# Kernel tuning notes

Hardware: AMD Instinct MI355X
Metric: run time of the kernel (lower is better)

The kernel has to match this reference:

```python
import jax, jax.numpy as jnp
import numpy as np

N_NODES = 50000
N_EDGES = 400000
D_PROT = 512
D_TEXT = 2048
GN_EPS = 1e-5


def setup_inputs() -> dict:
    key = jax.random.key(0)
    ks = jax.random.split(key, 8)
    s = 0.02
    return {
        "x": jax.random.normal(ks[0], (N_NODES, D_PROT), jnp.float32),
        "edge_index": jax.random.randint(ks[1], (2, N_EDGES), 0, N_NODES, dtype=jnp.int32),
        "gn_weight": jnp.ones((D_PROT,), jnp.float32),
        "gn_bias": jnp.zeros((D_PROT,), jnp.float32),
        "gn_mean_scale": jnp.ones((D_PROT,), jnp.float32),
        "conv1_w": jax.random.normal(ks[2], (D_PROT, D_PROT), jnp.float32) * s,
        "conv1_b": jnp.zeros((D_PROT,), jnp.float32),
        "conv2_w": jax.random.normal(ks[3], (D_PROT, D_PROT), jnp.float32) * s,
        "conv2_b": jnp.zeros((D_PROT,), jnp.float32),
        "proj1_w": jax.random.normal(ks[4], (D_TEXT, D_PROT), jnp.float32) * s,
        "proj1_b": jnp.zeros((D_TEXT,), jnp.float32),
        "proj2_w": jax.random.normal(ks[5], (D_TEXT, D_TEXT), jnp.float32) * s,
        "proj2_b": jnp.zeros((D_TEXT,), jnp.float32),
    }


def _graph_norm(x, weight, bias, mean_scale):
    # PyG GraphNorm over a single graph: shift by mean_scale*mean, scale by rstd
    mean = jnp.mean(x, axis=0, keepdims=True)            # [1, D]
    out = x - mean * mean_scale
    var = jnp.mean(out * out, axis=0, keepdims=True)     # [1, D]
    out = out * jax.lax.rsqrt(var + GN_EPS)
    return out * weight + bias


def _sgconv(x, src, dst, w, b):
    # SGConv K=1 with GCN normalization and added self-loops:
    n = x.shape[0]
    deg = jax.ops.segment_sum(jnp.ones_like(src, dtype=x.dtype), dst, num_segments=n) + 1.0
    dinv = jax.lax.rsqrt(deg)                            # [N]
    norm = dinv[src] * dinv[dst]                         # [E]
    agg = jax.ops.segment_sum(x[src] * norm[:, None], dst, num_segments=n)
    agg = agg + x * (dinv * dinv)[:, None]               # self-loop contribution
    return agg @ w.T + b


def reference(x, edge_index, gn_weight, gn_bias, gn_mean_scale,
              conv1_w, conv1_b, conv2_w, conv2_b,
              proj1_w, proj1_b, proj2_w, proj2_b):
    src, dst = edge_index[0], edge_index[1]
    h = _graph_norm(x, gn_weight, gn_bias, gn_mean_scale)
    h = jax.nn.relu(_sgconv(h, src, dst, conv1_w, conv1_b))  # dropout = identity (eval)
    h = jax.nn.relu(_sgconv(h, src, dst, conv2_w, conv2_b))
    h = h @ proj1_w.T + proj1_b
    h = jax.nn.gelu(h, approximate=False)
    h = h @ proj2_w.T + proj2_b
    return h
```

## Files before the change

### kernel.cpp

```cpp
#include <hip/hip_runtime.h>
#include <math.h>

typedef _Float16 half_t;
typedef _Float16 f16x2 __attribute__((ext_vector_type(2)));
typedef _Float16 f16x4 __attribute__((ext_vector_type(4)));
typedef _Float16 f16x8 __attribute__((ext_vector_type(8)));
typedef float f32x4 __attribute__((ext_vector_type(4)));

#define D_PROT 512
#define D_TEXT 2048

__global__ void k_cvt4(const float* __restrict__ s, half_t* __restrict__ d, int n4) {
    int i = blockIdx.x * 256 + threadIdx.x;
    if (i < n4) {
        float4 v = ((const float4*)s)[i];
        f16x4 o;
        o.x = (_Float16)v.x; o.y = (_Float16)v.y;
        o.z = (_Float16)v.z; o.w = (_Float16)v.w;
        ((f16x4*)d)[i] = o;
    }
}

__global__ void k_deg(const int* __restrict__ dst, int E, int* __restrict__ deg) {
    int i = blockIdx.x * 256 + threadIdx.x;
    if (i < E) atomicAdd(&deg[dst[i]], 1);
}

__global__ void k_dinv(const int* __restrict__ deg, float* __restrict__ dinv, int n) {
    int i = blockIdx.x * 256 + threadIdx.x;
    if (i < n) dinv[i] = rsqrtf((float)deg[i] + 1.0f);
}

__global__ void k_blocksum(const int* __restrict__ deg, int* __restrict__ bsum, int n) {
    __shared__ int sd[256];
    int i = blockIdx.x * 256 + threadIdx.x;
    sd[threadIdx.x] = (i < n) ? deg[i] : 0;
    __syncthreads();
    for (int s = 128; s > 0; s >>= 1) {
        if (threadIdx.x < s) sd[threadIdx.x] += sd[threadIdx.x + s];
        __syncthreads();
    }
    if (threadIdx.x == 0) bsum[blockIdx.x] = sd[0];
}

__global__ void k_scan_bsum(const int* __restrict__ bsum, int* __restrict__ boff, int nb) {
    __shared__ int sd[1024];
    int t = threadIdx.x;
    for (int i = t; i < 1024; i += 256) sd[i] = (i < nb) ? bsum[i] : 0;
    __syncthreads();
    for (int s = 1; s < 1024; s <<= 1) {
        int vals[4];
#pragma unroll
        for (int k = 0; k < 4; k++) {
            int i = t + k * 256;
            vals[k] = (i >= s) ? sd[i - s] : 0;
        }
        __syncthreads();
#pragma unroll
        for (int k = 0; k < 4; k++) sd[t + k * 256] += vals[k];
        __syncthreads();
    }
    for (int i = t; i < nb; i += 256) boff[i] = (i > 0) ? sd[i - 1] : 0;
}

__global__ void k_scan_final(const int* __restrict__ deg, const int* __restrict__ boff,
                             int* __restrict__ rowptr, int n) {
    __shared__ int sd[256];
    int i = blockIdx.x * 256 + threadIdx.x;
    int v = (i < n) ? deg[i] : 0;
    sd[threadIdx.x] = v;
    __syncthreads();
    for (int s = 1; s < 256; s <<= 1) {
        int t2 = (threadIdx.x >= s) ? sd[threadIdx.x - s] : 0;
        __syncthreads();
        sd[threadIdx.x] += t2;
        __syncthreads();
    }
    if (i < n) rowptr[i + 1] = boff[blockIdx.x] + sd[threadIdx.x];
}

__global__ void k_fill(const int* __restrict__ src, const int* __restrict__ dst, int E,
                       const int* __restrict__ rowptr, int* __restrict__ fill,
                       int* __restrict__ colidx) {
    int i = blockIdx.x * 256 + threadIdx.x;
    if (i < E) {
        int d = dst[i];
        int pos = atomicAdd(&fill[d], 1);
        colidx[rowptr[d] + pos] = src[i];
    }
}

__global__ void k_gnreduce(const float* __restrict__ x, float* __restrict__ sums,
                           float* __restrict__ sumsq, int Nn) {
    int t = threadIdx.x;
    int c = t * 2;
    float s0 = 0, s1 = 0, q0 = 0, q1 = 0;
    for (int r = blockIdx.x; r < Nn; r += gridDim.x) {
        float2 v = *(const float2*)(x + (size_t)r * D_PROT + c);
        s0 += v.x; s1 += v.y; q0 += v.x * v.x; q1 += v.y * v.y;
    }
    atomicAdd(&sums[c], s0);  atomicAdd(&sums[c + 1], s1);
    atomicAdd(&sumsq[c], q0); atomicAdd(&sumsq[c + 1], q1);
}

__global__ void k_gnfinal(const float* __restrict__ sums, const float* __restrict__ sumsq,
                          const float* __restrict__ w, const float* __restrict__ b,
                          const float* __restrict__ ms, float* __restrict__ ab, float invN) {
    int d = blockIdx.x * 256 + threadIdx.x;
    if (d < D_PROT) {
        float mean = sums[d] * invN;
        float m2 = sumsq[d] * invN;
        float mm = mean * ms[d];
        float var = m2 - 2.f * mm * mean + mm * mm;
        float rstd = rsqrtf(var + 1e-5f);
        float a = rstd * w[d];
        ab[d] = a;
        ab[D_PROT + d] = b[d] - mm * a;
    }
}

__global__ void k_gnnorm(const float* __restrict__ x, const float* __restrict__ ab,
                         half_t* __restrict__ h, int n4) {
    int i = blockIdx.x * 256 + threadIdx.x;
    if (i < n4) {
        size_t idx = (size_t)i * 4;
        float4 v = *(const float4*)(x + idx);
        int d = (int)(idx & (D_PROT - 1));
        const float* a = ab;
        const float* bb = ab + D_PROT;
        f16x4 o;
        o.x = (_Float16)(v.x * a[d]     + bb[d]);
        o.y = (_Float16)(v.y * a[d + 1] + bb[d + 1]);
        o.z = (_Float16)(v.z * a[d + 2] + bb[d + 2]);
        o.w = (_Float16)(v.w * a[d + 3] + bb[d + 3]);
        *(f16x4*)(h + idx) = o;
    }
}

__global__ void k_agg(const half_t* __restrict__ h, half_t* __restrict__ out,
                      const int* __restrict__ rowptr, const int* __restrict__ colidx,
                      const float* __restrict__ dinv, int Nn) {
    int wid = (blockIdx.x << 2) + (threadIdx.x >> 6);
    if (wid >= Nn) return;
    int lane = threadIdx.x & 63;
    int node = wid;
    float di = dinv[node];
    int beg = rowptr[node], end = rowptr[node + 1];
    const f16x8* hp = (const f16x8*)h;
    f16x8 sv = hp[(size_t)node * 64 + lane];
    float dii = di * di;
    float a[8];
#pragma unroll
    for (int j = 0; j < 8; j++) a[j] = (float)sv[j] * dii;
    int e = beg;
    for (; e + 4 <= end; e += 4) {
        int s0 = colidx[e],     s1 = colidx[e + 1];
        int s2 = colidx[e + 2], s3 = colidx[e + 3];
        float w0 = dinv[s0] * di, w1 = dinv[s1] * di;
        float w2 = dinv[s2] * di, w3 = dinv[s3] * di;
        f16x8 v0 = hp[(size_t)s0 * 64 + lane];
        f16x8 v1 = hp[(size_t)s1 * 64 + lane];
        f16x8 v2 = hp[(size_t)s2 * 64 + lane];
        f16x8 v3 = hp[(size_t)s3 * 64 + lane];
#pragma unroll
        for (int j = 0; j < 8; j++)
            a[j] += w0 * (float)v0[j] + w1 * (float)v1[j]
                  + w2 * (float)v2[j] + w3 * (float)v3[j];
    }
    for (; e < end; ++e) {
        int s = colidx[e];
        float wg = dinv[s] * di;
        f16x8 v = hp[(size_t)s * 64 + lane];
#pragma unroll
        for (int j = 0; j < 8; j++) a[j] += wg * (float)v[j];
    }
    f16x8 o;
#pragma unroll
    for (int j = 0; j < 8; j++) o[j] = (_Float16)a[j];
    ((f16x8*)out)[(size_t)node * 64 + lane] = o;
}

#define FENCE() asm volatile("" ::: "memory")
#define BAR()   do { FENCE(); __builtin_amdgcn_s_barrier(); FENCE(); } while (0)
#define WAITV4() asm volatile("s_waitcnt vmcnt(4)" ::: "memory")
#define WAITV0() asm volatile("s_waitcnt vmcnt(0)" ::: "memory")
#define GLD(src, dst) __builtin_amdgcn_global_load_lds( \
    (const __attribute__((address_space(1))) void*)(src), \
    (__attribute__((address_space(3))) void*)(dst), 16, 0, 0)
#define LDF(base, row, kk) \
    (*(const f16x8*)((base) + ((((row) * 128 + (kk) * 64 + fqo)) ^ (((row) & 7) << 4))))
#define MM(mi, nj, A_, B_) \
    acc[mi][nj] = __builtin_amdgcn_mfma_f32_16x16x32_f16(A_, B_, acc[mi][nj], 0, 0, 0)

template <int ACT, typename OUT_T>
__global__ __launch_bounds__(512, 2) void k_gemm8(const half_t* __restrict__ A,
                                                  const half_t* __restrict__ W,
                                                  const float* __restrict__ bias,
                                                  OUT_T* __restrict__ C,
                                                  int M, int N, int K) {
    __shared__ half_t sm[2][32768];
    const int gx = gridDim.x;
    const int nwg = gx * gridDim.y;
    int b = blockIdx.y * gx + blockIdx.x;
    int w8 = ((nwg & 7) == 0) ? (b & 7) * (nwg >> 3) + (b >> 3) : b;
    const int bn = (w8 % gx) * 256;
    const int bm = (w8 / gx) * 256;

    const int t = threadIdx.x;
    const int w = t >> 6, lane = t & 63;
    const int fr = lane & 15, fq = lane >> 4;
    const int fqo = fq * 16;
    const int wm = (w >> 2) * 128, wn = (w & 3) * 64;
    const int NT = K >> 6;

    int q0 = w * 512 + lane * 8;
    int q1 = 4096 + q0;
    int s0 = q0 ^ (((q0 >> 6) & 7) << 3);
    int s1 = q1 ^ (((q1 >> 6) & 7) << 3);
    int r0 = s0 >> 6, c0 = s0 & 63;
    int r1 = s1 >> 6, c1 = s1 & 63;
    const half_t* gAlo0 = A + (size_t)min(bm + r0, M - 1) * K + c0;
    const half_t* gAlo1 = A + (size_t)min(bm + r1, M - 1) * K + c1;
    const half_t* gAhi0 = A + (size_t)min(bm + 128 + r0, M - 1) * K + c0;
    const half_t* gAhi1 = A + (size_t)min(bm + 128 + r1, M - 1) * K + c1;
    const half_t* gBlo0 = W + (size_t)(bn + r0) * K + c0;
    const half_t* gBlo1 = W + (size_t)(bn + r1) * K + c1;
    const half_t* gBhi0 = W + (size_t)(bn + 128 + r0) * K + c0;
    const half_t* gBhi1 = W + (size_t)(bn + 128 + r1) * K + c1;
    const int dst0 = w * 512;

    f32x4 acc[8][4] = {};

    GLD(gAlo0, &sm[0][dst0]);          GLD(gAlo1, &sm[0][4096 + dst0]);
    GLD(gAhi0, &sm[0][8192 + dst0]);   GLD(gAhi1, &sm[0][12288 + dst0]);
    GLD(gBlo0, &sm[0][16384 + dst0]);  GLD(gBlo1, &sm[0][20480 + dst0]);
    GLD(gBhi0, &sm[0][24576 + dst0]);  GLD(gBhi1, &sm[0][28672 + dst0]);
    GLD(gBlo0 + 64, &sm[1][16384 + dst0]);  GLD(gBlo1 + 64, &sm[1][20480 + dst0]);
    GLD(gBhi0 + 64, &sm[1][24576 + dst0]);  GLD(gBhi1 + 64, &sm[1][28672 + dst0]);
    WAITV4();
    BAR();

#define TILE(cur, nxt, ktA, ktB) do {                                          \
    const char* smA = (const char*)&sm[cur][0];                                 \
    const char* smB = (const char*)&sm[cur][16384];                             \
                  \
    f16x8 b00 = LDF(smB, wn + fr, 0),      b01 = LDF(smB, wn + fr, 1);          \
    f16x8 b10 = LDF(smB, wn + 16 + fr, 0), b11 = LDF(smB, wn + 16 + fr, 1);     \
    f16x8 b20 = LDF(smB, wn + 32 + fr, 0), b21 = LDF(smB, wn + 32 + fr, 1);     \
    f16x8 b30 = LDF(smB, wn + 48 + fr, 0), b31 = LDF(smB, wn + 48 + fr, 1);     \
    f16x8 a00 = LDF(smA, wm + fr, 0),      a01 = LDF(smA, wm + fr, 1);          \
    f16x8 a10 = LDF(smA, wm + 16 + fr, 0), a11 = LDF(smA, wm + 16 + fr, 1);     \
    GLD(gAlo0 + (size_t)(ktA) * 64, &sm[nxt][dst0]);                            \
    GLD(gAlo1 + (size_t)(ktA) * 64, &sm[nxt][4096 + dst0]);                     \
    GLD(gAhi0 + (size_t)(ktA) * 64, &sm[nxt][8192 + dst0]);                     \
    GLD(gAhi1 + (size_t)(ktA) * 64, &sm[nxt][12288 + dst0]);                    \
    BAR();                                                                      \
    __builtin_amdgcn_s_setprio(1);                                              \
    MM(0, 0, a00, b00); MM(0, 1, a00, b10); MM(0, 2, a00, b20); MM(0, 3, a00, b30); \
    MM(0, 0, a01, b01); MM(0, 1, a01, b11); MM(0, 2, a01, b21); MM(0, 3, a01, b31); \
    MM(1, 0, a10, b00); MM(1, 1, a10, b10); MM(1, 2, a10, b20); MM(1, 3, a10, b30); \
    MM(1, 0, a11, b01); MM(1, 1, a11, b11); MM(1, 2, a11, b21); MM(1, 3, a11, b31); \
    __builtin_amdgcn_s_setprio(0);                                              \
    BAR();                                                                      \
                              \
    f16x8 a20 = LDF(smA, wm + 32 + fr, 0), a21 = LDF(smA, wm + 32 + fr, 1);     \
    f16x8 a30 = LDF(smA, wm + 48 + fr, 0), a31 = LDF(smA, wm + 48 + fr, 1);     \
    GLD(gBlo0 + (size_t)(ktB) * 64, &sm[cur][16384 + dst0]);                    \
    GLD(gBlo1 + (size_t)(ktB) * 64, &sm[cur][20480 + dst0]);                    \
    BAR();                                                                      \
    __builtin_amdgcn_s_setprio(1);                                              \
    MM(2, 0, a20, b00); MM(2, 1, a20, b10); MM(2, 2, a20, b20); MM(2, 3, a20, b30); \
    MM(2, 0, a21, b01); MM(2, 1, a21, b11); MM(2, 2, a21, b21); MM(2, 3, a21, b31); \
    MM(3, 0, a30, b00); MM(3, 1, a30, b10); MM(3, 2, a30, b20); MM(3, 3, a30, b30); \
    MM(3, 0, a31, b01); MM(3, 1, a31, b11); MM(3, 2, a31, b21); MM(3, 3, a31, b31); \
    __builtin_amdgcn_s_setprio(0);                                              \
    BAR();                                                                      \
                              \
    f16x8 a40 = LDF(smA, wm + 64 + fr, 0), a41 = LDF(smA, wm + 64 + fr, 1);     \
    f16x8 a50 = LDF(smA, wm + 80 + fr, 0), a51 = LDF(smA, wm + 80 + fr, 1);     \
    GLD(gBhi0 + (size_t)(ktB) * 64, &sm[cur][24576 + dst0]);                    \
    GLD(gBhi1 + (size_t)(ktB) * 64, &sm[cur][28672 + dst0]);                    \
    BAR();                                                                      \
    __builtin_amdgcn_s_setprio(1);                                              \
    MM(4, 0, a40, b00); MM(4, 1, a40, b10); MM(4, 2, a40, b20); MM(4, 3, a40, b30); \
    MM(4, 0, a41, b01); MM(4, 1, a41, b11); MM(4, 2, a41, b21); MM(4, 3, a41, b31); \
    MM(5, 0, a50, b00); MM(5, 1, a50, b10); MM(5, 2, a50, b20); MM(5, 3, a50, b30); \
    MM(5, 0, a51, b01); MM(5, 1, a51, b11); MM(5, 2, a51, b21); MM(5, 3, a51, b31); \
    __builtin_amdgcn_s_setprio(0);                                              \
    BAR();                                                                      \
                                       \
    f16x8 a60 = LDF(smA, wm + 96 + fr, 0),  a61 = LDF(smA, wm + 96 + fr, 1);    \
    f16x8 a70 = LDF(smA, wm + 112 + fr, 0), a71 = LDF(smA, wm + 112 + fr, 1);   \
    BAR();                                                                      \
    __builtin_amdgcn_s_setprio(1);                                              \
    MM(6, 0, a60, b00); MM(6, 1, a60, b10); MM(6, 2, a60, b20); MM(6, 3, a60, b30); \
    MM(6, 0, a61, b01); MM(6, 1, a61, b11); MM(6, 2, a61, b21); MM(6, 3, a61, b31); \
    MM(7, 0, a70, b00); MM(7, 1, a70, b10); MM(7, 2, a70, b20); MM(7, 3, a70, b30); \
    MM(7, 0, a71, b01); MM(7, 1, a71, b11); MM(7, 2, a71, b21); MM(7, 3, a71, b31); \
    __builtin_amdgcn_s_setprio(0);                                              \
    WAITV4();                                                                   \
    BAR();                                                                      \
} while (0)

    for (int tt = 0; tt < NT; tt += 2) {
        int kb1 = (tt + 2 < NT) ? tt + 2 : NT - 1;
        TILE(0, 1, tt + 1, kb1);
        int ka2 = (tt + 2 < NT) ? tt + 2 : NT - 1;
        int kb2 = (tt + 3 < NT) ? tt + 3 : NT - 1;
        TILE(1, 0, ka2, kb2);
    }
    WAITV0();
#undef TILE

    const int col0 = bn + wn + fr;
#pragma unroll
    for (int mi = 0; mi < 8; mi++) {
        int rb = bm + wm + mi * 16 + fq * 4;
#pragma unroll
        for (int nj = 0; nj < 4; nj++) {
            int col = col0 + nj * 16;
            float bv = bias[col];
#pragma unroll
            for (int r = 0; r < 4; r++) {
                int row = rb + r;
                if (row < M) {
                    float v = acc[mi][nj][r] + bv;
                    if (ACT == 1) v = fmaxf(v, 0.f);
                    if (ACT == 2) v = 0.5f * v * (1.f + erff(v * 0.70710678118f));
                    C[(size_t)row * N + col] = (OUT_T)v;
                }
            }
        }
    }
}

extern "C" void kernel_launch(void* const* d_in, const int* in_sizes, int n_in,
                              void* d_out, int out_size, void* d_ws, size_t ws_size,
                              hipStream_t stream) {
    const float* x     = (const float*)d_in[0];
    const int*   eidx  = (const int*)d_in[1];
    const float* gn_w  = (const float*)d_in[2];
    const float* gn_b  = (const float*)d_in[3];
    const float* gn_ms = (const float*)d_in[4];
    const float* w1    = (const float*)d_in[5];
    const float* b1    = (const float*)d_in[6];
    const float* w2    = (const float*)d_in[7];
    const float* b2    = (const float*)d_in[8];
    const float* p1    = (const float*)d_in[9];
    const float* pb1   = (const float*)d_in[10];
    const float* p2    = (const float*)d_in[11];
    const float* pb2   = (const float*)d_in[12];

    const int Nn = in_sizes[0] / D_PROT;
    const int E  = in_sizes[1] / 2;
    const int M  = Nn;

    char* ws = (char*)d_ws;
    size_t off = 0;
    auto alloc = [&](size_t bytes) {
        void* p = ws + off;
        off += (bytes + 255) & ~(size_t)255;
        return p;
    };
    half_t* w1h    = (half_t*)alloc((size_t)D_PROT * D_PROT * 2);
    half_t* w2h    = (half_t*)alloc((size_t)D_PROT * D_PROT * 2);
    half_t* p1h    = (half_t*)alloc((size_t)D_TEXT * D_PROT * 2);
    half_t* p2h    = (half_t*)alloc((size_t)D_TEXT * D_TEXT * 2);
    int*    deg    = (int*)alloc((size_t)Nn * 4);
    float*  dinv   = (float*)alloc((size_t)Nn * 4);
    int*    rowptr = (int*)alloc((size_t)(Nn + 1) * 4);
    int*    fillc  = (int*)alloc((size_t)Nn * 4);
    int*    bsum   = (int*)alloc(4096);
    int*    boff   = (int*)alloc(4096);
    int*    colidx = (int*)alloc((size_t)E * 4);
    float*  sums   = (float*)alloc(D_PROT * 4);
    float*  sumsq  = (float*)alloc(D_PROT * 4);
    float*  gnab   = (float*)alloc(2 * D_PROT * 4);
    half_t* buf1   = (half_t*)alloc((size_t)Nn * D_PROT * 2);
    half_t* buf2   = (half_t*)alloc((size_t)Nn * D_PROT * 2);
    half_t* big    = (half_t*)alloc((size_t)Nn * D_TEXT * 2);

    const int* esrc = eidx;
    const int* edst = eidx + E;

    hipMemsetAsync(deg, 0, (size_t)Nn * 4, stream);
    hipMemsetAsync(fillc, 0, (size_t)Nn * 4, stream);
    hipMemsetAsync(rowptr, 0, (size_t)(Nn + 1) * 4, stream);
    hipMemsetAsync(sums, 0, D_PROT * 4, stream);
    hipMemsetAsync(sumsq, 0, D_PROT * 4, stream);

    k_cvt4<<<(D_PROT * D_PROT / 4 + 255) / 256, 256, 0, stream>>>(w1, w1h, D_PROT * D_PROT / 4);
    k_cvt4<<<(D_PROT * D_PROT / 4 + 255) / 256, 256, 0, stream>>>(w2, w2h, D_PROT * D_PROT / 4);
    k_cvt4<<<(D_TEXT * D_PROT / 4 + 255) / 256, 256, 0, stream>>>(p1, p1h, D_TEXT * D_PROT / 4);
    k_cvt4<<<(D_TEXT * D_TEXT / 4 + 255) / 256, 256, 0, stream>>>(p2, p2h, D_TEXT * D_TEXT / 4);

    int eb = (E + 255) / 256;
    int nb = (Nn + 255) / 256;
    k_deg<<<eb, 256, 0, stream>>>(edst, E, deg);
    k_dinv<<<nb, 256, 0, stream>>>(deg, dinv, Nn);
    k_blocksum<<<nb, 256, 0, stream>>>(deg, bsum, Nn);
    k_scan_bsum<<<1, 256, 0, stream>>>(bsum, boff, nb);
    k_scan_final<<<nb, 256, 0, stream>>>(deg, boff, rowptr, Nn);
    k_fill<<<eb, 256, 0, stream>>>(esrc, edst, E, rowptr, fillc, colidx);

    k_gnreduce<<<256, 256, 0, stream>>>(x, sums, sumsq, Nn);
    k_gnfinal<<<2, 256, 0, stream>>>(sums, sumsq, gn_w, gn_b, gn_ms, gnab, 1.0f / (float)Nn);
    int n4 = Nn * D_PROT / 4;
    k_gnnorm<<<(n4 + 255) / 256, 256, 0, stream>>>(x, gnab, buf1, n4);

    const int mt256 = (M + 255) / 256;
    const int aggb = (Nn + 3) / 4;

    k_agg<<<aggb, 256, 0, stream>>>(buf1, buf2, rowptr, colidx, dinv, Nn);
    {
        dim3 g(D_PROT / 256, mt256);
        k_gemm8<1, half_t><<<g, 512, 0, stream>>>(buf2, w1h, b1, buf1, M, D_PROT, D_PROT);
    }
    k_agg<<<aggb, 256, 0, stream>>>(buf1, buf2, rowptr, colidx, dinv, Nn);
    {
        dim3 g(D_PROT / 256, mt256);
        k_gemm8<1, half_t><<<g, 512, 0, stream>>>(buf2, w2h, b2, buf1, M, D_PROT, D_PROT);
    }
    {
        dim3 g(D_TEXT / 256, mt256);
        k_gemm8<2, half_t><<<g, 512, 0, stream>>>(buf1, p1h, pb1, big, M, D_TEXT, D_PROT);
    }
    {
        dim3 g(D_TEXT / 256, mt256);
        k_gemm8<0, float><<<g, 512, 0, stream>>>(big, p2h, pb2, (float*)d_out, M, D_TEXT, D_TEXT);
    }
}
```

Baseline: 1.249 ms.

## Restructure GEMM to 256x128 tiles with K=32 triple-buffered LDS pipeline

Rewrites the fp16 MFMA GEMM from 256x256 tiles with K=64 double buffering to 256x128 tiles with K=32 steps and a three-stage LDS ring. It uses a new swizzle, a simpler per-iteration loop with one barrier, and a column-major workgroup order that walks M inside each N strip. Less LDS per block and launch_bounds raised to 4 are meant to give higher occupancy and a deeper prefetch. In exchange, each block reuses less data per MFMA and B tiles are reloaded more often, so global and LDS traffic per FLOP rises.

```diff
diff --git a/kernel.cpp b/kernel.cpp
--- a/kernel.cpp
+++ b/kernel.cpp
@@ -2,7 +2,6 @@
 #include <math.h>
 
 typedef _Float16 half_t;
-typedef _Float16 f16x2 __attribute__((ext_vector_type(2)));
 typedef _Float16 f16x4 __attribute__((ext_vector_type(4)));
 typedef _Float16 f16x8 __attribute__((ext_vector_type(8)));
 typedef float f32x4 __attribute__((ext_vector_type(4)));
@@ -182,149 +181,97 @@
 
 #define FENCE() asm volatile("" ::: "memory")
 #define BAR()   do { FENCE(); __builtin_amdgcn_s_barrier(); FENCE(); } while (0)
-#define WAITV4() asm volatile("s_waitcnt vmcnt(4)" ::: "memory")
+#define WAITV3() asm volatile("s_waitcnt vmcnt(3)" ::: "memory")
 #define WAITV0() asm volatile("s_waitcnt vmcnt(0)" ::: "memory")
 #define GLD(src, dst) __builtin_amdgcn_global_load_lds( \
     (const __attribute__((address_space(1))) void*)(src), \
     (__attribute__((address_space(3))) void*)(dst), 16, 0, 0)
-#define LDF(base, row, kk) \
-    (*(const f16x8*)((base) + ((((row) * 128 + (kk) * 64 + fqo)) ^ (((row) & 7) << 4))))
+#define LDF(base, row) \
+    (*(const f16x8*)((base) + ((((row) * 64 + fqo)) ^ ((((row) >> 1) & 3) << 4))))
 #define MM(mi, nj, A_, B_) \
     acc[mi][nj] = __builtin_amdgcn_mfma_f32_16x16x32_f16(A_, B_, acc[mi][nj], 0, 0, 0)
 
 template <int ACT, typename OUT_T>
-__global__ __launch_bounds__(512, 2) void k_gemm8(const half_t* __restrict__ A,
+__global__ __launch_bounds__(512, 4) void k_gemm8(const half_t* __restrict__ A,
                                                   const half_t* __restrict__ W,
                                                   const float* __restrict__ bias,
                                                   OUT_T* __restrict__ C,
                                                   int M, int N, int K) {
-    __shared__ half_t sm[2][32768];
+    __shared__ half_t sm[36864];
     const int gx = gridDim.x;
-    const int nwg = gx * gridDim.y;
+    const int mt = gridDim.y;
+    const int nwg = gx * mt;
     int b = blockIdx.y * gx + blockIdx.x;
     int w8 = ((nwg & 7) == 0) ? (b & 7) * (nwg >> 3) + (b >> 3) : b;
-    const int bn = (w8 % gx) * 256;
-    const int bm = (w8 / gx) * 256;
+    const int bn = (w8 / mt) * 128;
+    const int bm = (w8 % mt) * 256;
 
     const int t = threadIdx.x;
     const int w = t >> 6, lane = t & 63;
     const int fr = lane & 15, fq = lane >> 4;
     const int fqo = fq * 16;
-    const int wm = (w >> 2) * 128, wn = (w & 3) * 64;
-    const int NT = K >> 6;
-
-    int q0 = w * 512 + lane * 8;
-    int q1 = 4096 + q0;
-    int s0 = q0 ^ (((q0 >> 6) & 7) << 3);
-    int s1 = q1 ^ (((q1 >> 6) & 7) << 3);
-    int r0 = s0 >> 6, c0 = s0 & 63;
-    int r1 = s1 >> 6, c1 = s1 & 63;
-    const half_t* gAlo0 = A + (size_t)min(bm + r0, M - 1) * K + c0;
-    const half_t* gAlo1 = A + (size_t)min(bm + r1, M - 1) * K + c1;
-    const half_t* gAhi0 = A + (size_t)min(bm + 128 + r0, M - 1) * K + c0;
-    const half_t* gAhi1 = A + (size_t)min(bm + 128 + r1, M - 1) * K + c1;
-    const half_t* gBlo0 = W + (size_t)(bn + r0) * K + c0;
-    const half_t* gBlo1 = W + (size_t)(bn + r1) * K + c1;
-    const half_t* gBhi0 = W + (size_t)(bn + 128 + r0) * K + c0;
-    const half_t* gBhi1 = W + (size_t)(bn + 128 + r1) * K + c1;
+    const int wm = (w >> 1) * 64, wn = (w & 1) * 64;
+    const int NT = K >> 5;
+
+    int q = w * 512 + lane * 8;
+    int s = q ^ (((q >> 6) & 3) << 3);
+    int r = s >> 5, c = s & 31;
+    const half_t* gAlo = A + (size_t)min(bm + r, M - 1) * K + c;
+    const half_t* gAhi = A + (size_t)min(bm + 128 + r, M - 1) * K + c;
+    const half_t* gB   = W + (size_t)(bn + r) * K + c;
     const int dst0 = w * 512;
 
-    f32x4 acc[8][4] = {};
-
-    GLD(gAlo0, &sm[0][dst0]);          GLD(gAlo1, &sm[0][4096 + dst0]);
-    GLD(gAhi0, &sm[0][8192 + dst0]);   GLD(gAhi1, &sm[0][12288 + dst0]);
-    GLD(gBlo0, &sm[0][16384 + dst0]);  GLD(gBlo1, &sm[0][20480 + dst0]);
-    GLD(gBhi0, &sm[0][24576 + dst0]);  GLD(gBhi1, &sm[0][28672 + dst0]);
-    GLD(gBlo0 + 64, &sm[1][16384 + dst0]);  GLD(gBlo1 + 64, &sm[1][20480 + dst0]);
-    GLD(gBhi0 + 64, &sm[1][24576 + dst0]);  GLD(gBhi1 + 64, &sm[1][28672 + dst0]);
-    WAITV4();
+#define STAGE(b3, kt) do {                                                     \
+    GLD(gB   + (size_t)(kt) * 32, &sm[(b3) * 12288 + 8192 + dst0]);            \
+    GLD(gAlo + (size_t)(kt) * 32, &sm[(b3) * 12288 + dst0]);                   \
+    GLD(gAhi + (size_t)(kt) * 32, &sm[(b3) * 12288 + 4096 + dst0]);            \
+} while (0)
+
+    f32x4 acc[4][4] = {};
+
+    STAGE(0, 0);
+    STAGE(1, (NT > 1) ? 1 : 0);
+    WAITV3();
     BAR();
 
-#define TILE(cur, nxt, ktA, ktB) do {                                          \
-    const char* smA = (const char*)&sm[cur][0];                                 \
-    const char* smB = (const char*)&sm[cur][16384];                             \
-                  \
-    f16x8 b00 = LDF(smB, wn + fr, 0),      b01 = LDF(smB, wn + fr, 1);          \
-    f16x8 b10 = LDF(smB, wn + 16 + fr, 0), b11 = LDF(smB, wn + 16 + fr, 1);     \
-    f16x8 b20 = LDF(smB, wn + 32 + fr, 0), b21 = LDF(smB, wn + 32 + fr, 1);     \
-    f16x8 b30 = LDF(smB, wn + 48 + fr, 0), b31 = LDF(smB, wn + 48 + fr, 1);     \
-    f16x8 a00 = LDF(smA, wm + fr, 0),      a01 = LDF(smA, wm + fr, 1);          \
-    f16x8 a10 = LDF(smA, wm + 16 + fr, 0), a11 = LDF(smA, wm + 16 + fr, 1);     \
-    GLD(gAlo0 + (size_t)(ktA) * 64, &sm[nxt][dst0]);                            \
-    GLD(gAlo1 + (size_t)(ktA) * 64, &sm[nxt][4096 + dst0]);                     \
-    GLD(gAhi0 + (size_t)(ktA) * 64, &sm[nxt][8192 + dst0]);                     \
-    GLD(gAhi1 + (size_t)(ktA) * 64, &sm[nxt][12288 + dst0]);                    \
-    BAR();                                                                      \
-    __builtin_amdgcn_s_setprio(1);                                              \
-    MM(0, 0, a00, b00); MM(0, 1, a00, b10); MM(0, 2, a00, b20); MM(0, 3, a00, b30); \
-    MM(0, 0, a01, b01); MM(0, 1, a01, b11); MM(0, 2, a01, b21); MM(0, 3, a01, b31); \
-    MM(1, 0, a10, b00); MM(1, 1, a10, b10); MM(1, 2, a10, b20); MM(1, 3, a10, b30); \
-    MM(1, 0, a11, b01); MM(1, 1, a11, b11); MM(1, 2, a11, b21); MM(1, 3, a11, b31); \
-    __builtin_amdgcn_s_setprio(0);                                              \
-    BAR();                                                                      \
-                              \
-    f16x8 a20 = LDF(smA, wm + 32 + fr, 0), a21 = LDF(smA, wm + 32 + fr, 1);     \
-    f16x8 a30 = LDF(smA, wm + 48 + fr, 0), a31 = LDF(smA, wm + 48 + fr, 1);     \
-    GLD(gBlo0 + (size_t)(ktB) * 64, &sm[cur][16384 + dst0]);                    \
-    GLD(gBlo1 + (size_t)(ktB) * 64, &sm[cur][20480 + dst0]);                    \
-    BAR();                                                                      \
-    __builtin_amdgcn_s_setprio(1);                                              \
-    MM(2, 0, a20, b00); MM(2, 1, a20, b10); MM(2, 2, a20, b20); MM(2, 3, a20, b30); \
-    MM(2, 0, a21, b01); MM(2, 1, a21, b11); MM(2, 2, a21, b21); MM(2, 3, a21, b31); \
-    MM(3, 0, a30, b00); MM(3, 1, a30, b10); MM(3, 2, a30, b20); MM(3, 3, a30, b30); \
-    MM(3, 0, a31, b01); MM(3, 1, a31, b11); MM(3, 2, a31, b21); MM(3, 3, a31, b31); \
-    __builtin_amdgcn_s_setprio(0);                                              \
-    BAR();                                                                      \
-                              \
-    f16x8 a40 = LDF(smA, wm + 64 + fr, 0), a41 = LDF(smA, wm + 64 + fr, 1);     \
-    f16x8 a50 = LDF(smA, wm + 80 + fr, 0), a51 = LDF(smA, wm + 80 + fr, 1);     \
-    GLD(gBhi0 + (size_t)(ktB) * 64, &sm[cur][24576 + dst0]);                    \
-    GLD(gBhi1 + (size_t)(ktB) * 64, &sm[cur][28672 + dst0]);                    \
-    BAR();                                                                      \
-    __builtin_amdgcn_s_setprio(1);                                              \
-    MM(4, 0, a40, b00); MM(4, 1, a40, b10); MM(4, 2, a40, b20); MM(4, 3, a40, b30); \
-    MM(4, 0, a41, b01); MM(4, 1, a41, b11); MM(4, 2, a41, b21); MM(4, 3, a41, b31); \
-    MM(5, 0, a50, b00); MM(5, 1, a50, b10); MM(5, 2, a50, b20); MM(5, 3, a50, b30); \
-    MM(5, 0, a51, b01); MM(5, 1, a51, b11); MM(5, 2, a51, b21); MM(5, 3, a51, b31); \
-    __builtin_amdgcn_s_setprio(0);                                              \
-    BAR();                                                                      \
-                                       \
-    f16x8 a60 = LDF(smA, wm + 96 + fr, 0),  a61 = LDF(smA, wm + 96 + fr, 1);    \
-    f16x8 a70 = LDF(smA, wm + 112 + fr, 0), a71 = LDF(smA, wm + 112 + fr, 1);   \
-    BAR();                                                                      \
-    __builtin_amdgcn_s_setprio(1);                                              \
-    MM(6, 0, a60, b00); MM(6, 1, a60, b10); MM(6, 2, a60, b20); MM(6, 3, a60, b30); \
-    MM(6, 0, a61, b01); MM(6, 1, a61, b11); MM(6, 2, a61, b21); MM(6, 3, a61, b31); \
-    MM(7, 0, a70, b00); MM(7, 1, a70, b10); MM(7, 2, a70, b20); MM(7, 3, a70, b30); \
-    MM(7, 0, a71, b01); MM(7, 1, a71, b11); MM(7, 2, a71, b21); MM(7, 3, a71, b31); \
-    __builtin_amdgcn_s_setprio(0);                                              \
-    WAITV4();                                                                   \
-    BAR();                                                                      \
-} while (0)
-
-    for (int tt = 0; tt < NT; tt += 2) {
-        int kb1 = (tt + 2 < NT) ? tt + 2 : NT - 1;
-        TILE(0, 1, tt + 1, kb1);
-        int ka2 = (tt + 2 < NT) ? tt + 2 : NT - 1;
-        int kb2 = (tt + 3 < NT) ? tt + 3 : NT - 1;
-        TILE(1, 0, ka2, kb2);
+    for (int tt = 0; tt < NT; ++tt) {
+        const int cur = tt % 3;
+        const int s2 = (tt + 2) % 3;
+        const int kt = (tt + 2 < NT) ? tt + 2 : NT - 1;
+        const char* smA = (const char*)&sm[cur * 12288];
+        const char* smB = smA + 16384;
+        STAGE(s2, kt);
+        f16x8 b0 = LDF(smB, wn + fr);
+        f16x8 b1 = LDF(smB, wn + 16 + fr);
+        f16x8 b2 = LDF(smB, wn + 32 + fr);
+        f16x8 b3 = LDF(smB, wn + 48 + fr);
+        __builtin_amdgcn_s_setprio(1);
+#pragma unroll
+        for (int mi = 0; mi < 4; mi++) {
+            f16x8 a = LDF(smA, wm + mi * 16 + fr);
+            MM(mi, 0, a, b0); MM(mi, 1, a, b1);
+            MM(mi, 2, a, b2); MM(mi, 3, a, b3);
+        }
+        __builtin_amdgcn_s_setprio(0);
+        WAITV3();
+        BAR();
     }
     WAITV0();
-#undef TILE
+#undef STAGE
 
     const int col0 = bn + wn + fr;
 #pragma unroll
-    for (int mi = 0; mi < 8; mi++) {
+    for (int mi = 0; mi < 4; mi++) {
         int rb = bm + wm + mi * 16 + fq * 4;
 #pragma unroll
         for (int nj = 0; nj < 4; nj++) {
             int col = col0 + nj * 16;
             float bv = bias[col];
 #pragma unroll
-            for (int r = 0; r < 4; r++) {
-                int row = rb + r;
+            for (int rr = 0; rr < 4; rr++) {
+                int row = rb + rr;
                 if (row < M) {
-                    float v = acc[mi][nj][r] + bv;
+                    float v = acc[mi][nj][rr] + bv;
                     if (ACT == 1) v = fmaxf(v, 0.f);
                     if (ACT == 2) v = 0.5f * v * (1.f + erff(v * 0.70710678118f));
                     C[(size_t)row * N + col] = (OUT_T)v;
@@ -413,20 +360,20 @@
 
     k_agg<<<aggb, 256, 0, stream>>>(buf1, buf2, rowptr, colidx, dinv, Nn);
     {
-        dim3 g(D_PROT / 256, mt256);
+        dim3 g(D_PROT / 128, mt256);
         k_gemm8<1, half_t><<<g, 512, 0, stream>>>(buf2, w1h, b1, buf1, M, D_PROT, D_PROT);
     }
     k_agg<<<aggb, 256, 0, stream>>>(buf1, buf2, rowptr, colidx, dinv, Nn);
     {
-        dim3 g(D_PROT / 256, mt256);
+        dim3 g(D_PROT / 128, mt256);
         k_gemm8<1, half_t><<<g, 512, 0, stream>>>(buf2, w2h, b2, buf1, M, D_PROT, D_PROT);
     }
     {
-        dim3 g(D_TEXT / 256, mt256);
+        dim3 g(D_TEXT / 128, mt256);
         k_gemm8<2, half_t><<<g, 512, 0, stream>>>(buf1, p1h, pb1, big, M, D_TEXT, D_PROT);
     }
     {
-        dim3 g(D_TEXT / 256, mt256);
+        dim3 g(D_TEXT / 128, mt256);
         k_gemm8<0, float><<<g, 512, 0, stream>>>(big, p2h, pb2, (float*)d_out, M, D_TEXT, D_TEXT);
     }
 }
```

After: 1.289 ms. 3.3% more time.

## Add 256x128 triple-buffered GEMM kernel for small-K layers

Applied to the files above, without the earlier changes.

Adds a new GEMM kernel with a 256x128 output tile, K-step of 32, a three-stage LDS ring buffer and launch bounds allowing four blocks per CU. It is used for the two 512x512 conv GEMMs and the 512->2048 projection, while the large 2048x2048 projection keeps the existing 256x256 kernel (renamed). The aim is more workgroups and better latency hiding when K is small, at the cost of lower per-tile data reuse and more barriers per unit of work.

```diff
diff --git a/kernel.cpp b/kernel.cpp
--- a/kernel.cpp
+++ b/kernel.cpp
@@ -2,7 +2,6 @@
 #include <math.h>
 
 typedef _Float16 half_t;
-typedef _Float16 f16x2 __attribute__((ext_vector_type(2)));
 typedef _Float16 f16x4 __attribute__((ext_vector_type(4)));
 typedef _Float16 f16x8 __attribute__((ext_vector_type(8)));
 typedef float f32x4 __attribute__((ext_vector_type(4)));
@@ -183,21 +182,23 @@
 #define FENCE() asm volatile("" ::: "memory")
 #define BAR()   do { FENCE(); __builtin_amdgcn_s_barrier(); FENCE(); } while (0)
 #define WAITV4() asm volatile("s_waitcnt vmcnt(4)" ::: "memory")
+#define WAITV3() asm volatile("s_waitcnt vmcnt(3)" ::: "memory")
 #define WAITV0() asm volatile("s_waitcnt vmcnt(0)" ::: "memory")
 #define GLD(src, dst) __builtin_amdgcn_global_load_lds( \
     (const __attribute__((address_space(1))) void*)(src), \
     (__attribute__((address_space(3))) void*)(dst), 16, 0, 0)
-#define LDF(base, row, kk) \
-    (*(const f16x8*)((base) + ((((row) * 128 + (kk) * 64 + fqo)) ^ (((row) & 7) << 4))))
 #define MM(mi, nj, A_, B_) \
     acc[mi][nj] = __builtin_amdgcn_mfma_f32_16x16x32_f16(A_, B_, acc[mi][nj], 0, 0, 0)
 
+#define LDF256(base, row, kk) \
+    (*(const f16x8*)((base) + ((((row) * 128 + (kk) * 64 + fqo)) ^ (((row) & 7) << 4))))
+
 template <int ACT, typename OUT_T>
-__global__ __launch_bounds__(512, 2) void k_gemm8(const half_t* __restrict__ A,
-                                                  const half_t* __restrict__ W,
-                                                  const float* __restrict__ bias,
-                                                  OUT_T* __restrict__ C,
-                                                  int M, int N, int K) {
+__global__ __launch_bounds__(512, 2) void k_gemm256(const half_t* __restrict__ A,
+                                                    const half_t* __restrict__ W,
+                                                    const float* __restrict__ bias,
+                                                    OUT_T* __restrict__ C,
+                                                    int M, int N, int K) {
     __shared__ half_t sm[2][32768];
     const int gx = gridDim.x;
     const int nwg = gx * gridDim.y;
@@ -243,13 +244,12 @@
 #define TILE(cur, nxt, ktA, ktB) do {                                          \
     const char* smA = (const char*)&sm[cur][0];                                 \
     const char* smB = (const char*)&sm[cur][16384];                             \
-                  \
-    f16x8 b00 = LDF(smB, wn + fr, 0),      b01 = LDF(smB, wn + fr, 1);          \
-    f16x8 b10 = LDF(smB, wn + 16 + fr, 0), b11 = LDF(smB, wn + 16 + fr, 1);     \
-    f16x8 b20 = LDF(smB, wn + 32 + fr, 0), b21 = LDF(smB, wn + 32 + fr, 1);     \
-    f16x8 b30 = LDF(smB, wn + 48 + fr, 0), b31 = LDF(smB, wn + 48 + fr, 1);     \
-    f16x8 a00 = LDF(smA, wm + fr, 0),      a01 = LDF(smA, wm + fr, 1);          \
-    f16x8 a10 = LDF(smA, wm + 16 + fr, 0), a11 = LDF(smA, wm + 16 + fr, 1);     \
+    f16x8 b00 = LDF256(smB, wn + fr, 0),      b01 = LDF256(smB, wn + fr, 1);    \
+    f16x8 b10 = LDF256(smB, wn + 16 + fr, 0), b11 = LDF256(smB, wn + 16 + fr, 1); \
+    f16x8 b20 = LDF256(smB, wn + 32 + fr, 0), b21 = LDF256(smB, wn + 32 + fr, 1); \
+    f16x8 b30 = LDF256(smB, wn + 48 + fr, 0), b31 = LDF256(smB, wn + 48 + fr, 1); \
+    f16x8 a00 = LDF256(smA, wm + fr, 0),      a01 = LDF256(smA, wm + fr, 1);    \
+    f16x8 a10 = LDF256(smA, wm + 16 + fr, 0), a11 = LDF256(smA, wm + 16 + fr, 1); \
     GLD(gAlo0 + (size_t)(ktA) * 64, &sm[nxt][dst0]);                            \
     GLD(gAlo1 + (size_t)(ktA) * 64, &sm[nxt][4096 + dst0]);                     \
     GLD(gAhi0 + (size_t)(ktA) * 64, &sm[nxt][8192 + dst0]);                     \
@@ -262,9 +262,8 @@
     MM(1, 0, a11, b01); MM(1, 1, a11, b11); MM(1, 2, a11, b21); MM(1, 3, a11, b31); \
     __builtin_amdgcn_s_setprio(0);                                              \
     BAR();                                                                      \
-                              \
-    f16x8 a20 = LDF(smA, wm + 32 + fr, 0), a21 = LDF(smA, wm + 32 + fr, 1);     \
-    f16x8 a30 = LDF(smA, wm + 48 + fr, 0), a31 = LDF(smA, wm + 48 + fr, 1);     \
+    f16x8 a20 = LDF256(smA, wm + 32 + fr, 0), a21 = LDF256(smA, wm + 32 + fr, 1); \
+    f16x8 a30 = LDF256(smA, wm + 48 + fr, 0), a31 = LDF256(smA, wm + 48 + fr, 1); \
     GLD(gBlo0 + (size_t)(ktB) * 64, &sm[cur][16384 + dst0]);                    \
     GLD(gBlo1 + (size_t)(ktB) * 64, &sm[cur][20480 + dst0]);                    \
     BAR();                                                                      \
@@ -275,9 +274,8 @@
     MM(3, 0, a31, b01); MM(3, 1, a31, b11); MM(3, 2, a31, b21); MM(3, 3, a31, b31); \
     __builtin_amdgcn_s_setprio(0);                                              \
     BAR();                                                                      \
-                              \
-    f16x8 a40 = LDF(smA, wm + 64 + fr, 0), a41 = LDF(smA, wm + 64 + fr, 1);     \
-    f16x8 a50 = LDF(smA, wm + 80 + fr, 0), a51 = LDF(smA, wm + 80 + fr, 1);     \
+    f16x8 a40 = LDF256(smA, wm + 64 + fr, 0), a41 = LDF256(smA, wm + 64 + fr, 1); \
+    f16x8 a50 = LDF256(smA, wm + 80 + fr, 0), a51 = LDF256(smA, wm + 80 + fr, 1); \
     GLD(gBhi0 + (size_t)(ktB) * 64, &sm[cur][24576 + dst0]);                    \
     GLD(gBhi1 + (size_t)(ktB) * 64, &sm[cur][28672 + dst0]);                    \
     BAR();                                                                      \
@@ -288,9 +286,8 @@
     MM(5, 0, a51, b01); MM(5, 1, a51, b11); MM(5, 2, a51, b21); MM(5, 3, a51, b31); \
     __builtin_amdgcn_s_setprio(0);                                              \
     BAR();                                                                      \
-                                       \
-    f16x8 a60 = LDF(smA, wm + 96 + fr, 0),  a61 = LDF(smA, wm + 96 + fr, 1);    \
-    f16x8 a70 = LDF(smA, wm + 112 + fr, 0), a71 = LDF(smA, wm + 112 + fr, 1);   \
+    f16x8 a60 = LDF256(smA, wm + 96 + fr, 0),  a61 = LDF256(smA, wm + 96 + fr, 1); \
+    f16x8 a70 = LDF256(smA, wm + 112 + fr, 0), a71 = LDF256(smA, wm + 112 + fr, 1); \
     BAR();                                                                      \
     __builtin_amdgcn_s_setprio(1);                                              \
     MM(6, 0, a60, b00); MM(6, 1, a60, b10); MM(6, 2, a60, b20); MM(6, 3, a60, b30); \
@@ -325,6 +322,98 @@
                 int row = rb + r;
                 if (row < M) {
                     float v = acc[mi][nj][r] + bv;
+                    if (ACT == 1) v = fmaxf(v, 0.f);
+                    if (ACT == 2) v = 0.5f * v * (1.f + erff(v * 0.70710678118f));
+                    C[(size_t)row * N + col] = (OUT_T)v;
+                }
+            }
+        }
+    }
+}
+
+#define LDF128(base, row) \
+    (*(const f16x8*)((base) + ((((row) * 64 + fqo)) ^ ((((row) >> 1) & 3) << 4))))
+
+template <int ACT, typename OUT_T>
+__global__ __launch_bounds__(512, 4) void k_gemm128(const half_t* __restrict__ A,
+                                                    const half_t* __restrict__ W,
+                                                    const float* __restrict__ bias,
+                                                    OUT_T* __restrict__ C,
+                                                    int M, int N, int K) {
+    __shared__ half_t sm[36864];
+    const int gx = gridDim.x;
+    const int nwg = gx * gridDim.y;
+    int b = blockIdx.y * gx + blockIdx.x;
+    int w8 = ((nwg & 7) == 0) ? (b & 7) * (nwg >> 3) + (b >> 3) : b;
+    const int bn = (w8 % gx) * 128;
+    const int bm = (w8 / gx) * 256;
+
+    const int t = threadIdx.x;
+    const int w = t >> 6, lane = t & 63;
+    const int fr = lane & 15, fq = lane >> 4;
+    const int fqo = fq * 16;
+    const int wm = (w >> 1) * 64, wn = (w & 1) * 64;
+    const int NT = K >> 5;
+
+    int q = w * 512 + lane * 8;
+    int s = q ^ (((q >> 6) & 3) << 3);
+    int r = s >> 5, c = s & 31;
+    const half_t* gAlo = A + (size_t)min(bm + r, M - 1) * K + c;
+    const half_t* gAhi = A + (size_t)min(bm + 128 + r, M - 1) * K + c;
+    const half_t* gB   = W + (size_t)(bn + r) * K + c;
+    const int dst0 = w * 512;
+
+#define STAGE(b3, kt) do {                                                     \
+    GLD(gB   + (size_t)(kt) * 32, &sm[(b3) * 12288 + 8192 + dst0]);            \
+    GLD(gAlo + (size_t)(kt) * 32, &sm[(b3) * 12288 + dst0]);                   \
+    GLD(gAhi + (size_t)(kt) * 32, &sm[(b3) * 12288 + 4096 + dst0]);            \
+} while (0)
+
+    f32x4 acc[4][4] = {};
+
+    STAGE(0, 0);
+    STAGE(1, (NT > 1) ? 1 : 0);
+    WAITV3();
+    BAR();
+
+    for (int tt = 0; tt < NT; ++tt) {
+        const int cur = tt % 3;
+        const int s2 = (tt + 2) % 3;
+        const int kt = (tt + 2 < NT) ? tt + 2 : NT - 1;
+        const char* smA = (const char*)&sm[cur * 12288];
+        const char* smB = smA + 16384;
+        STAGE(s2, kt);
+        f16x8 b0 = LDF128(smB, wn + fr);
+        f16x8 b1 = LDF128(smB, wn + 16 + fr);
+        f16x8 b2 = LDF128(smB, wn + 32 + fr);
+        f16x8 b3 = LDF128(smB, wn + 48 + fr);
+        __builtin_amdgcn_s_setprio(1);
+#pragma unroll
+        for (int mi = 0; mi < 4; mi++) {
+            f16x8 a = LDF128(smA, wm + mi * 16 + fr);
+            MM(mi, 0, a, b0); MM(mi, 1, a, b1);
+            MM(mi, 2, a, b2); MM(mi, 3, a, b3);
+        }
+        __builtin_amdgcn_s_setprio(0);
+        WAITV3();
+        BAR();
+    }
+    WAITV0();
+#undef STAGE
+
+    const int col0 = bn + wn + fr;
+#pragma unroll
+    for (int mi = 0; mi < 4; mi++) {
+        int rb = bm + wm + mi * 16 + fq * 4;
+#pragma unroll
+        for (int nj = 0; nj < 4; nj++) {
+            int col = col0 + nj * 16;
+            float bv = bias[col];
+#pragma unroll
+            for (int rr = 0; rr < 4; rr++) {
+                int row = rb + rr;
+                if (row < M) {
+                    float v = acc[mi][nj][rr] + bv;
                     if (ACT == 1) v = fmaxf(v, 0.f);
                     if (ACT == 2) v = 0.5f * v * (1.f + erff(v * 0.70710678118f));
                     C[(size_t)row * N + col] = (OUT_T)v;
@@ -413,20 +502,20 @@
 
     k_agg<<<aggb, 256, 0, stream>>>(buf1, buf2, rowptr, colidx, dinv, Nn);
     {
-        dim3 g(D_PROT / 256, mt256);
-        k_gemm8<1, half_t><<<g, 512, 0, stream>>>(buf2, w1h, b1, buf1, M, D_PROT, D_PROT);
+        dim3 g(D_PROT / 128, mt256);
+        k_gemm128<1, half_t><<<g, 512, 0, stream>>>(buf2, w1h, b1, buf1, M, D_PROT, D_PROT);
     }
     k_agg<<<aggb, 256, 0, stream>>>(buf1, buf2, rowptr, colidx, dinv, Nn);
     {
-        dim3 g(D_PROT / 256, mt256);
-        k_gemm8<1, half_t><<<g, 512, 0, stream>>>(buf2, w2h, b2, buf1, M, D_PROT, D_PROT);
+        dim3 g(D_PROT / 128, mt256);
+        k_gemm128<1, half_t><<<g, 512, 0, stream>>>(buf2, w2h, b2, buf1, M, D_PROT, D_PROT);
+    }
+    {
+        dim3 g(D_TEXT / 128, mt256);
+        k_gemm128<2, half_t><<<g, 512, 0, stream>>>(buf1, p1h, pb1, big, M, D_TEXT, D_PROT);
     }
     {
         dim3 g(D_TEXT / 256, mt256);
-        k_gemm8<2, half_t><<<g, 512, 0, stream>>>(buf1, p1h, pb1, big, M, D_TEXT, D_PROT);
-    }
-    {
-        dim3 g(D_TEXT / 256, mt256);
-        k_gemm8<0, float><<<g, 512, 0, stream>>>(big, p2h, pb2, (float*)d_out, M, D_TEXT, D_TEXT);
-    }
-}
+        k_gemm256<0, float><<<g, 512, 0, stream>>>(big, p2h, pb2, (float*)d_out, M, D_TEXT, D_TEXT);
+    }
+}
```

After: 1.096 ms. -12.2%, faster.
